# Kernel tuning notes

Hardware: AMD Instinct MI355X
Metric: run time of the kernel (lower is better)

## Reference

```python
import jax, jax.numpy as jnp
import numpy as np

B, N, D, T, L = 16, 64, 4, 40, 10
H, K = 128, 4
E = N * (N - 1)


def setup_inputs() -> dict:
    key = jax.random.key(0)
    ks = jax.random.split(key, 24)
    s = 0.05
    off = np.ones((N, N)) - np.eye(N)
    recv, send = np.where(off)  # rel_rec one-hot of recv, rel_send one-hot of send
    p = {}
    p["data"] = jax.random.normal(ks[0], (B, N, D, T), jnp.float32)
    p["rel_type"] = jax.random.uniform(ks[1], (B, E, K), dtype=jnp.float32)
    p["msg_W1"] = jax.random.normal(ks[2], (K, 2 * H, H), jnp.float32) * s
    p["msg_b1"] = jnp.zeros((K, H), jnp.float32)
    p["msg_W2"] = jax.random.normal(ks[3], (K, H, H), jnp.float32) * s
    p["msg_b2"] = jnp.zeros((K, H), jnp.float32)
    p["Wr_h"] = jax.random.normal(ks[4], (H, H), jnp.float32) * s
    p["Wi_h"] = jax.random.normal(ks[5], (H, H), jnp.float32) * s
    p["Wh_h"] = jax.random.normal(ks[6], (H, H), jnp.float32) * s
    p["Wr_in"] = jax.random.normal(ks[7], (D, H), jnp.float32) * s
    p["br_in"] = jnp.zeros((H,), jnp.float32)
    p["Wi_in"] = jax.random.normal(ks[8], (D, H), jnp.float32) * s
    p["bi_in"] = jnp.zeros((H,), jnp.float32)
    p["Wn_in"] = jax.random.normal(ks[9], (D, H), jnp.float32) * s
    p["bn_in"] = jnp.zeros((H,), jnp.float32)
    p["Wo1"] = jax.random.normal(ks[10], (H, H), jnp.float32) * s
    p["bo1"] = jnp.zeros((H,), jnp.float32)
    p["Wo2"] = jax.random.normal(ks[11], (H, H), jnp.float32) * s
    p["bo2"] = jnp.zeros((H,), jnp.float32)
    p["Wo3"] = jax.random.normal(ks[12], (H, D), jnp.float32) * s
    p["bo3"] = jnp.zeros((D,), jnp.float32)
    p["recv_idx"] = jnp.asarray(recv, jnp.int32)
    p["send_idx"] = jnp.asarray(send, jnp.int32)
    return p


def _forward(data, rel_type, msg_W1, msg_b1, msg_W2, msg_b2, Wr_h, Wi_h, Wh_h,
             Wr_in, br_in, Wi_in, bi_in, Wn_in, bn_in,
             Wo1, bo1, Wo2, bo2, Wo3, bo3, recv_idx, send_idx):
    inputs = jnp.transpose(data, (0, 3, 1, 2))  # [B,T,N,D]
    Bv = inputs.shape[0]

    def single_step(ins, hidden):
        # gather == matmul with one-hot rel_send / rel_rec
        pre_msg = jnp.concatenate([hidden[:, send_idx], hidden[:, recv_idx]], axis=-1)  # [B,E,2H]
        m = jnp.tanh(jnp.einsum('bef,kfh->bkeh', pre_msg, msg_W1) + msg_b1[None, :, None, :])
        m = jnp.tanh(jnp.einsum('bkeh,khg->bkeg', m, msg_W2) + msg_b2[None, :, None, :])
        # sum over edge types weighted by rel_type, normalized by num edge types
        all_msgs = jnp.einsum('bkeh,bek->beh', m, rel_type) / K
        # scatter-add to receivers == rel_rec^T matmul; normalized by n_in_node
        agg = jnp.zeros((Bv, N, H), all_msgs.dtype).at[:, recv_idx].add(all_msgs) / D
        r = jax.nn.sigmoid(ins @ Wr_in + br_in + agg @ Wr_h)
        i = jax.nn.sigmoid(ins @ Wi_in + bi_in + agg @ Wi_h)
        n = jnp.tanh(ins @ Wn_in + bn_in + r * (agg @ Wh_h))
        hidden = (1.0 - i) * n + i * hidden
        y = jax.nn.relu(hidden @ Wo1 + bo1)
        y = jax.nn.relu(y @ Wo2 + bo2)
        pred = ins + y @ Wo3 + bo3
        return pred, hidden

    inputs_pad = jnp.concatenate([inputs, jnp.zeros((Bv, L, N, D), inputs.dtype)], axis=1)
    xs_t = jnp.transpose(inputs_pad, (1, 0, 2, 3))  # [T+L,B,N,D]

    def scan_fn(carry, xs):
        hidden, prev = carry
        step, x_t = xs
        ins = jnp.where(step < T, x_t, prev)  # burn-in then closed-loop
        pred, hidden = single_step(ins, hidden)
        return (hidden, pred), pred

    init = (jnp.zeros((Bv, N, H), jnp.float32), jnp.zeros((Bv, N, D), jnp.float32))
    _, preds = jax.lax.scan(scan_fn, init, (jnp.arange(T + L), xs_t))
    preds = jnp.transpose(preds, (1, 2, 3, 0))  # [B,N,D,T+L]
    return preds[..., -L:]


def reference(data, rel_type, msg_W1, msg_b1, msg_W2, msg_b2, Wr_h, Wi_h, Wh_h,
              Wr_in, br_in, Wi_in, bi_in, Wn_in, bn_in,
              Wo1, bo1, Wo2, bo2, Wo3, bo3, recv_idx, send_idx):
    return _forward(data, rel_type, msg_W1, msg_b1, msg_W2, msg_b2, Wr_h, Wi_h, Wh_h,
                    Wr_in, br_in, Wi_in, bi_in, Wn_in, bn_in,
                    Wo1, bo1, Wo2, bo2, Wo3, bo3, recv_idx, send_idx)
```

## Files before the change

### kernel.cpp

```cpp
#include <hip/hip_runtime.h>
#include <hip/hip_bf16.h>
#include <math.h>

#define Bb 16
#define Nn 64
#define Dd 4
#define Tt 40
#define Ll 10
#define Hh 128
#define Kk 4
#define Ee (Nn*(Nn-1))
#define BNH (Bb*Nn*Hh)
#define SIGMA 2.8853900817779268f

typedef __attribute__((ext_vector_type(8))) short short8;
typedef __attribute__((ext_vector_type(4))) float f32x4;

#define AS1 __attribute__((address_space(1)))
#define AS3 __attribute__((address_space(3)))

__device__ __forceinline__ float tanhE(float y){
    float e = __builtin_amdgcn_exp2f(y);
    float r = __builtin_amdgcn_rcpf(e + 1.0f);
    return fmaf(-2.0f, r, 1.0f);
}
__device__ __forceinline__ float tanh_fast(float x){ return tanhE(SIGMA * x); }
__device__ __forceinline__ float sigmoid_fast(float x){
    return __builtin_amdgcn_rcpf(1.0f + __expf(-x));
}
__device__ __forceinline__ unsigned short f2bf(float x){
    unsigned int u = __float_as_uint(x);
    return (unsigned short)((u + 0x7FFFu + ((u >> 16) & 1u)) >> 16);
}
__device__ __forceinline__ unsigned int pack_bf2(float lo, float hi){
    union { __hip_bfloat162 h; unsigned int u; } cv;
    cv.h = __float22bfloat162_rn(make_float2(lo, hi));
    return cv.u;
}
__device__ __forceinline__ void g2lds16(const void* g, void* l){
    __builtin_amdgcn_global_load_lds((const AS1 unsigned int*)g,
                                     (AS3 unsigned int*)l, 16, 0, 0);
}

__global__ void __launch_bounds__(256) kW2f(const float* __restrict__ W2,
                                            const float* __restrict__ b2,
                                            unsigned short* __restrict__ W2f,
                                            float* __restrict__ b2l){
    if (blockIdx.x == 32){
        int i = threadIdx.x;
        b2l[i]       = SIGMA * b2[i];
        b2l[i + 256] = SIGMA * b2[i + 256];
        return;
    }
    int t    = blockIdx.x * 256 + threadIdx.x;
    int lane = t & 63;
    int nt   = (t >> 6) & 7;
    int kc   = (t >> 9) & 3;
    int k    = (t >> 11) & 3;
    int col  = nt * 16 + (lane & 15);
    int fb   = kc * 32 + (lane >> 4) * 8;
    unsigned int w[4];
#pragma unroll
    for (int p = 0; p < 4; ++p){
        unsigned short lo = f2bf(W2[(k*Hh + fb + 2*p    )*Hh + col]);
        unsigned short hi = f2bf(W2[(k*Hh + fb + 2*p + 1)*Hh + col]);
        w[p] = (unsigned int)lo | ((unsigned int)hi << 16);
    }
    ((uint4*)W2f)[t] = make_uint4(w[0], w[1], w[2], w[3]);
}

__global__ void __launch_bounds__(256) kW1f(const float* __restrict__ W1,
                                            unsigned short* __restrict__ W1f){
    int t    = blockIdx.x * 256 + threadIdx.x;
    int lane = t & 63;
    int nt   = (t >> 6) & 7;
    int kc   = (t >> 9) & 3;
    int s    = t >> 11;
    int col  = nt * 16 + (lane & 15);
    int fb   = kc * 32 + (lane >> 4) * 8;
    unsigned int w[4];
#pragma unroll
    for (int p = 0; p < 4; ++p){
        unsigned short lo = f2bf(W1[(size_t)(s*Hh + fb + 2*p    )*Hh + col]);
        unsigned short hi = f2bf(W1[(size_t)(s*Hh + fb + 2*p + 1)*Hh + col]);
        w[p] = (unsigned int)lo | ((unsigned int)hi << 16);
    }
    ((uint4*)W1f)[t] = make_uint4(w[0], w[1], w[2], w[3]);
}

__global__ void __launch_bounds__(256) kInit(const float* __restrict__ b1,
                                             float* __restrict__ Sf,
                                             float* __restrict__ Rr){
    int i = blockIdx.x*256 + threadIdx.x;
    Sf[i] = 0.0f;
    Rr[i] = SIGMA * b1[((i >> 13) & 3)*Hh + (i & 127)];
}

__global__ void __launch_bounds__(256) kA(const unsigned short* __restrict__ hbf,
                                          const unsigned short* __restrict__ W1f,
                                          const float* __restrict__ b1,
                                          float* __restrict__ Sf,
                                          float* __restrict__ Rr){
    const int blk   = blockIdx.x;
    const int bk    = blk & 63;
    const int b     = bk >> 2;
    const int k     = bk & 3;
    const int inner = blk >> 6;
    const int sr    = inner >> 1;
    const int mh    = inner & 1;
    const int s     = k*2 + sr;
    const int tid  = threadIdx.x;
    const int wave = tid >> 6;
    const int lane = tid & 63;
    const int nt0  = wave * 2;

    const short8* hv = (const short8*)hbf;
    const short8* wv = (const short8*)W1f;

    short8 a[2][4], bf[2][4];
#pragma unroll
    for (int m = 0; m < 2; ++m)
#pragma unroll
        for (int kc = 0; kc < 4; ++kc)
            a[m][kc] = hv[((size_t)((b*4 + mh*2 + m)*4) + kc)*64 + lane];
#pragma unroll
    for (int n = 0; n < 2; ++n)
#pragma unroll
        for (int kc = 0; kc < 4; ++kc)
            bf[n][kc] = wv[((size_t)(s*4 + kc)*8 + nt0 + n)*64 + lane];

    f32x4 acc[2][2];
#pragma unroll
    for (int m = 0; m < 2; ++m){ acc[m][0] = (f32x4)0.0f; acc[m][1] = (f32x4)0.0f; }

#pragma unroll
    for (int kc = 0; kc < 4; ++kc)
#pragma unroll
        for (int m = 0; m < 2; ++m){
            acc[m][0] = __builtin_amdgcn_mfma_f32_16x16x32_bf16(a[m][kc], bf[0][kc], acc[m][0], 0, 0, 0);
            acc[m][1] = __builtin_amdgcn_mfma_f32_16x16x32_bf16(a[m][kc], bf[1][kc], acc[m][1], 0, 0, 0);
        }

    const int col = lane & 15;
    const int r0  = (lane >> 4) << 2;
#pragma unroll
    for (int n = 0; n < 2; ++n){
        const int h  = (nt0 + n)*16 + col;
        const float bv = (sr == 1) ? b1[k*Hh + h] : 0.0f;
#pragma unroll
        for (int m = 0; m < 2; ++m){
            const int Mt = mh*2 + m;
#pragma unroll
            for (int r = 0; r < 4; ++r){
                const int node = Mt*16 + r0 + r;
                const float v = SIGMA*(acc[m][n][r] + bv);
                if (sr == 0)
                    Sf[((size_t)((b*4+k)*16 + (h>>3)))*512 + node*8 + (h&7)] = v;
                else
                    Rr[((size_t)((b*4+k)*64 + node))*128 + h] = v;
            }
        }
    }
}

__global__ void __launch_bounds__(256) kB(const float* __restrict__ Sf,
                                          const float* __restrict__ Rr,
                                          const unsigned short* __restrict__ W2f,
                                          const float* __restrict__ b2l,
                                          const float* __restrict__ rel,
                                          const int*   __restrict__ send_idx,
                                          float* __restrict__ aggp){
    __shared__ unsigned short w2s[32*512];
    __shared__ float rel_s[4][64];
    __shared__ float b2s[Hh];
    __shared__ float redu[4][4][Hh];

    const int blk  = blockIdx.x;
    const int bk   = blk & 63;
    const int nq   = blk >> 6;
    const int b    = bk >> 2;
    const int k    = bk & 3;
    const int n0   = nq * 4;
    const int tid  = threadIdx.x;
    const int wave = tid >> 6;
    const int lane = tid & 63;

    {
        const uint4* src = (const uint4*)(W2f + (size_t)k*16384);
        uint4* dst = (uint4*)w2s;
#pragma unroll
        for (int i = 0; i < 8; ++i)
            g2lds16(src + tid + i*256, dst + tid + i*256);
    }
    {
        int g = tid >> 6, e = tid & 63;
        rel_s[g][e] = (e < 63) ? rel[(b*Ee + (n0+g)*63 + e)*Kk + k] : 0.0f;
    }
    if (tid < 128) b2s[tid] = b2l[k*Hh + tid];
    __syncthreads();

    const int e  = wave*16 + (lane & 15);
    const int fo = lane >> 4;
    const float* SfB = Sf + (size_t)((b*4 + k)*16)*512;

    const int re   = wave*16 + ((lane >> 4) << 2);
    const int colb = lane & 15;
    const short8* w2v = (const short8*)w2s;

#pragma unroll
    for (int ph = 0; ph < 2; ++ph){
        short8 a0[4], a1[4];
#pragma unroll
        for (int n = 0; n < 2; ++n){
            const int nn = n0 + ph*2 + n;
            int srow = 0; if (e < 63) srow = send_idx[nn*63 + e];
            const float* Rp = Rr + (size_t)((b*4 + k)*64 + nn)*128;
#pragma unroll
            for (int kc = 0; kc < 4; ++kc){
                const int fg = kc*4 + fo;
                const float4* sv = (const float4*)(SfB + fg*512 + srow*8);
                const float4* rv = (const float4*)(Rp + fg*8);
                float4 s0 = sv[0], s1 = sv[1];
                float4 r0 = rv[0], r1 = rv[1];
                union { short8 v; unsigned int u[4]; } av;
                av.u[0] = pack_bf2(tanhE(s0.x+r0.x), tanhE(s0.y+r0.y));
                av.u[1] = pack_bf2(tanhE(s0.z+r0.z), tanhE(s0.w+r0.w));
                av.u[2] = pack_bf2(tanhE(s1.x+r1.x), tanhE(s1.y+r1.y));
                av.u[3] = pack_bf2(tanhE(s1.z+r1.z), tanhE(s1.w+r1.w));
                if (n == 0) a0[kc] = av.v; else a1[kc] = av.v;
            }
        }

        f32x4 acc0[8], acc1[8];
#pragma unroll
        for (int nt = 0; nt < 8; ++nt){ acc0[nt] = (f32x4)0.0f; acc1[nt] = (f32x4)0.0f; }
#pragma unroll
        for (int kc = 0; kc < 4; ++kc){
#pragma unroll
            for (int nt = 0; nt < 8; ++nt){
                short8 bfr = w2v[(kc*8 + nt)*64 + lane];
                acc0[nt] = __builtin_amdgcn_mfma_f32_16x16x32_bf16(a0[kc], bfr, acc0[nt], 0, 0, 0);
                acc1[nt] = __builtin_amdgcn_mfma_f32_16x16x32_bf16(a1[kc], bfr, acc1[nt], 0, 0, 0);
            }
        }

#pragma unroll
        for (int n = 0; n < 2; ++n){
            const float* relp = rel_s[ph*2 + n];
#pragma unroll
            for (int nt = 0; nt < 8; ++nt){
                f32x4 ac = (n == 0) ? acc0[nt] : acc1[nt];
                float bv = b2s[nt*16 + colb];
                float s = 0.0f;
#pragma unroll
                for (int r = 0; r < 4; ++r)
                    s = fmaf(relp[re + r], tanhE(fmaf(SIGMA, ac[r], bv)), s);
                s += __shfl_xor(s, 16);
                s += __shfl_xor(s, 32);
                if (lane < 16) redu[wave][ph*2 + n][nt*16 + lane] = s;
            }
        }
    }

    __syncthreads();
#pragma unroll
    for (int i = 0; i < 2; ++i){
        int idx = tid + i*256;
        int rcv = idx >> 7, h = idx & 127;
        float v = redu[0][rcv][h] + redu[1][rcv][h] + redu[2][rcv][h] + redu[3][rcv][h];
        aggp[(size_t)k*BNH + (size_t)(b*64 + n0 + rcv)*Hh + h] = v;
    }
}

__global__ void __launch_bounds__(128) kC(const float* __restrict__ data,
                                          const float* __restrict__ aggp,
                                          float* __restrict__ hidden,
                                          float* __restrict__ prevpred,
                                          unsigned short* __restrict__ hbf,
                                          const float* __restrict__ Wr_in, const float* __restrict__ br_in,
                                          const float* __restrict__ Wi_in, const float* __restrict__ bi_in,
                                          const float* __restrict__ Wn_in, const float* __restrict__ bn_in,
                                          const float* __restrict__ Wr_h,  const float* __restrict__ Wi_h,
                                          const float* __restrict__ Wh_h,
                                          const float* __restrict__ Wo1,   const float* __restrict__ bo1,
                                          const float* __restrict__ Wo2,   const float* __restrict__ bo2,
                                          const float* __restrict__ Wo3,   const float* __restrict__ bo3,
                                          float* __restrict__ out, int t){
    __shared__ float aggL[4][Hh];
    __shared__ float buf[4][Hh];
    __shared__ float insL[4][Dd];

    const int bn0 = blockIdx.x * 4;
    const int h   = threadIdx.x;

#pragma unroll
    for (int g = 0; g < 4; ++g){
        int bn = bn0 + g;
        aggL[g][h] = (aggp[bn*Hh + h] + aggp[BNH + bn*Hh + h] +
                      aggp[2*BNH + bn*Hh + h] + aggp[3*BNH + bn*Hh + h]) * (1.0f/16.0f);
    }
    if (h < 16){
        int g = h >> 2, d = h & 3;
        int bn = bn0 + g;
        insL[g][d] = (t < Tt) ? data[(bn*Dd + d)*Tt + t] : prevpred[bn*Dd + d];
    }
    __syncthreads();

    float rh[4] = {0,0,0,0}, ih[4] = {0,0,0,0}, hh[4] = {0,0,0,0};
    for (int f = 0; f < Hh; ++f){
        float wr = Wr_h[f*Hh + h], wi = Wi_h[f*Hh + h], wh = Wh_h[f*Hh + h];
#pragma unroll
        for (int g = 0; g < 4; ++g){
            float av = aggL[g][f];
            rh[g] += av*wr; ih[g] += av*wi; hh[g] += av*wh;
        }
    }

    const float wr0 = Wr_in[h],        wr1 = Wr_in[Hh + h],
                wr2 = Wr_in[2*Hh + h], wr3 = Wr_in[3*Hh + h];
    const float wi0 = Wi_in[h],        wi1 = Wi_in[Hh + h],
                wi2 = Wi_in[2*Hh + h], wi3 = Wi_in[3*Hh + h];
    const float wn0 = Wn_in[h],        wn1 = Wn_in[Hh + h],
                wn2 = Wn_in[2*Hh + h], wn3 = Wn_in[3*Hh + h];
    const float brv = br_in[h], biv = bi_in[h], bnv = bn_in[h];

    const int kc  = h >> 5;
    const int lhi = (h >> 3) & 3;
    const int j   = h & 7;

#pragma unroll
    for (int g = 0; g < 4; ++g){
        float i0 = insL[g][0], i1 = insL[g][1], i2 = insL[g][2], i3 = insL[g][3];
        float r  = sigmoid_fast(brv + i0*wr0 + i1*wr1 + i2*wr2 + i3*wr3 + rh[g]);
        float ii = sigmoid_fast(biv + i0*wi0 + i1*wi1 + i2*wi2 + i3*wi3 + ih[g]);
        float nn = tanh_fast   (bnv + i0*wn0 + i1*wn1 + i2*wn2 + i3*wn3 + r*hh[g]);
        float hold = hidden[(bn0+g)*Hh + h];
        float hnew = (1.0f - ii)*nn + ii*hold;
        hidden[(bn0+g)*Hh + h] = hnew;
        buf[g][h] = hnew;
        int bn   = bn0 + g;
        int bb   = bn >> 6, node64 = bn & 63;
        int Mt   = node64 >> 4;
        int lane = (node64 & 15) + lhi*16;
        hbf[((size_t)((bb*4 + Mt)*4 + kc)*64 + lane)*8 + j] = f2bf(hnew);
    }
    __syncthreads();

    float y1[4]; const float b1v = bo1[h];
#pragma unroll
    for (int g = 0; g < 4; ++g) y1[g] = b1v;
    for (int f = 0; f < Hh; ++f){
        float wv = Wo1[f*Hh + h];
#pragma unroll
        for (int g = 0; g < 4; ++g) y1[g] += buf[g][f]*wv;
    }
    __syncthreads();
#pragma unroll
    for (int g = 0; g < 4; ++g) buf[g][h] = fmaxf(y1[g], 0.0f);
    __syncthreads();

    float y2[4]; const float b2v = bo2[h];
#pragma unroll
    for (int g = 0; g < 4; ++g) y2[g] = b2v;
    for (int f = 0; f < Hh; ++f){
        float wv = Wo2[f*Hh + h];
#pragma unroll
        for (int g = 0; g < 4; ++g) y2[g] += buf[g][f]*wv;
    }
    __syncthreads();
#pragma unroll
    for (int g = 0; g < 4; ++g) buf[g][h] = fmaxf(y2[g], 0.0f);
    __syncthreads();

    if (h < 16){
        int g = h >> 2, d = h & 3;
        float pv = bo3[d];
        for (int f = 0; f < Hh; ++f) pv += buf[g][f]*Wo3[f*Dd + d];
        pv += insL[g][d];
        int bn = bn0 + g;
        prevpred[bn*Dd + d] = pv;
        if (t >= Tt) out[(bn*Dd + d)*Ll + (t - Tt)] = pv;
    }
}

extern "C" void kernel_launch(void* const* d_in, const int* in_sizes, int n_in,
                              void* d_out, int out_size, void* d_ws, size_t ws_size,
                              hipStream_t stream){
    const float* data  = (const float*)d_in[0];
    const float* rel   = (const float*)d_in[1];
    const float* W1    = (const float*)d_in[2];
    const float* b1    = (const float*)d_in[3];
    const float* W2    = (const float*)d_in[4];
    const float* b2    = (const float*)d_in[5];
    const float* Wr_h  = (const float*)d_in[6];
    const float* Wi_h  = (const float*)d_in[7];
    const float* Wh_h  = (const float*)d_in[8];
    const float* Wr_in = (const float*)d_in[9];
    const float* br_in = (const float*)d_in[10];
    const float* Wi_in = (const float*)d_in[11];
    const float* bi_in = (const float*)d_in[12];
    const float* Wn_in = (const float*)d_in[13];
    const float* bn_in = (const float*)d_in[14];
    const float* Wo1   = (const float*)d_in[15];
    const float* bo1   = (const float*)d_in[16];
    const float* Wo2   = (const float*)d_in[17];
    const float* bo2   = (const float*)d_in[18];
    const float* Wo3   = (const float*)d_in[19];
    const float* bo3   = (const float*)d_in[20];
    const int* send_idx = (const int*)d_in[22];

    float* out = (float*)d_out;
    float* ws  = (float*)d_ws;

    float* hidden   = ws;
    float* prevpred = hidden + BNH;
    float* Sf       = prevpred + Bb*Nn*Dd;
    float* Rr       = Sf + Bb*Kk*16*Nn*8;
    float* aggp     = Rr + Bb*Kk*Nn*Hh;
    unsigned short* W2f = (unsigned short*)(aggp + 4*BNH);
    float* b2l      = (float*)(W2f + 65536);
    unsigned short* W1f = (unsigned short*)(b2l + 512);
    unsigned short* hbf = W1f + 131072;

    hipMemsetAsync(hidden, 0, (Bb*Nn*Hh + Bb*Nn*Dd)*sizeof(float), stream);
    kW2f<<<33, 256, 0, stream>>>(W2, b2, W2f, b2l);
    kW1f<<<64, 256, 0, stream>>>(W1, W1f);
    kInit<<<2048, 256, 0, stream>>>(b1, Sf, Rr);

    for (int t = 0; t < Tt + Ll; ++t){
        kB<<<1024, 256, 0, stream>>>(Sf, Rr, W2f, b2l, rel, send_idx, aggp);
        kC<<<256, 128, 0, stream>>>(data, aggp, hidden, prevpred, hbf,
                                    Wr_in, br_in, Wi_in, bi_in, Wn_in, bn_in,
                                    Wr_h, Wi_h, Wh_h,
                                    Wo1, bo1, Wo2, bo2, Wo3, bo3, out, t);
        if (t < Tt + Ll - 1)
            kA<<<256, 256, 0, stream>>>(hbf, W1f, b1, Sf, Rr);
    }
}
```

Baseline: 2.360 ms.

## Assign one receiver per wave in kB, dropping send_idx gather and LDS reduction

```diff
diff --git a/kernel.cpp b/kernel.cpp
--- a/kernel.cpp
+++ b/kernel.cpp
@@ -168,12 +168,10 @@
                                           const unsigned short* __restrict__ W2f,
                                           const float* __restrict__ b2l,
                                           const float* __restrict__ rel,
-                                          const int*   __restrict__ send_idx,
                                           float* __restrict__ aggp){
     __shared__ unsigned short w2s[32*512];
     __shared__ float rel_s[4][64];
     __shared__ float b2s[Hh];
-    __shared__ float redu[4][4][Hh];
 
     const int blk  = blockIdx.x;
     const int bk   = blk & 63;
@@ -193,82 +191,80 @@
             g2lds16(src + tid + i*256, dst + tid + i*256);
     }
     {
-        int g = tid >> 6, e = tid & 63;
-        rel_s[g][e] = (e < 63) ? rel[(b*Ee + (n0+g)*63 + e)*Kk + k] : 0.0f;
+        int g = tid >> 6, s = tid & 63;
+        int n = n0 + g;
+        float w = 0.0f;
+        if (s != n){
+            int e = s - (s > n);
+            w = rel[(b*Ee + n*63 + e)*Kk + k];
+        }
+        rel_s[g][s] = w;
     }
     if (tid < 128) b2s[tid] = b2l[k*Hh + tid];
     __syncthreads();
 
-    const int e  = wave*16 + (lane & 15);
-    const int fo = lane >> 4;
+    const int n    = n0 + wave;
+    const int fo   = lane >> 4;
+    const int srow = lane & 15;
     const float* SfB = Sf + (size_t)((b*4 + k)*16)*512;
-
-    const int re   = wave*16 + ((lane >> 4) << 2);
-    const int colb = lane & 15;
+    const float* Rp  = Rr + (size_t)((b*4 + k)*64 + n)*128;
     const short8* w2v = (const short8*)w2s;
-
-#pragma unroll
-    for (int ph = 0; ph < 2; ++ph){
-        short8 a0[4], a1[4];
-#pragma unroll
-        for (int n = 0; n < 2; ++n){
-            const int nn = n0 + ph*2 + n;
-            int srow = 0; if (e < 63) srow = send_idx[nn*63 + e];
-            const float* Rp = Rr + (size_t)((b*4 + k)*64 + nn)*128;
-#pragma unroll
-            for (int kc = 0; kc < 4; ++kc){
-                const int fg = kc*4 + fo;
-                const float4* sv = (const float4*)(SfB + fg*512 + srow*8);
-                const float4* rv = (const float4*)(Rp + fg*8);
-                float4 s0 = sv[0], s1 = sv[1];
-                float4 r0 = rv[0], r1 = rv[1];
-                union { short8 v; unsigned int u[4]; } av;
-                av.u[0] = pack_bf2(tanhE(s0.x+r0.x), tanhE(s0.y+r0.y));
-                av.u[1] = pack_bf2(tanhE(s0.z+r0.z), tanhE(s0.w+r0.w));
-                av.u[2] = pack_bf2(tanhE(s1.x+r1.x), tanhE(s1.y+r1.y));
-                av.u[3] = pack_bf2(tanhE(s1.z+r1.z), tanhE(s1.w+r1.w));
-                if (n == 0) a0[kc] = av.v; else a1[kc] = av.v;
-            }
-        }
-
-        f32x4 acc0[8], acc1[8];
-#pragma unroll
-        for (int nt = 0; nt < 8; ++nt){ acc0[nt] = (f32x4)0.0f; acc1[nt] = (f32x4)0.0f; }
+    const float* relw = rel_s[wave];
+
+    const int colb  = lane & 15;
+    const int rbase = (lane >> 4) << 2;
+
+    float aggacc[8];
+#pragma unroll
+    for (int nt = 0; nt < 8; ++nt) aggacc[nt] = 0.0f;
+
+#pragma unroll
+    for (int st = 0; st < 4; ++st){
+        short8 a[4];
+#pragma unroll
+        for (int kc = 0; kc < 4; ++kc){
+            const int fg = kc*4 + fo;
+            const float4* sv = (const float4*)(SfB + fg*512 + (st*16 + srow)*8);
+            const float4* rv = (const float4*)(Rp + fg*8);
+            float4 s0 = sv[0], s1 = sv[1];
+            float4 r0 = rv[0], r1 = rv[1];
+            union { short8 v; unsigned int u[4]; } av;
+            av.u[0] = pack_bf2(tanhE(s0.x+r0.x), tanhE(s0.y+r0.y));
+            av.u[1] = pack_bf2(tanhE(s0.z+r0.z), tanhE(s0.w+r0.w));
+            av.u[2] = pack_bf2(tanhE(s1.x+r1.x), tanhE(s1.y+r1.y));
+            av.u[3] = pack_bf2(tanhE(s1.z+r1.z), tanhE(s1.w+r1.w));
+            a[kc] = av.v;
+        }
+
+        f32x4 acc[8];
+#pragma unroll
+        for (int nt = 0; nt < 8; ++nt) acc[nt] = (f32x4)0.0f;
 #pragma unroll
         for (int kc = 0; kc < 4; ++kc){
 #pragma unroll
             for (int nt = 0; nt < 8; ++nt){
                 short8 bfr = w2v[(kc*8 + nt)*64 + lane];
-                acc0[nt] = __builtin_amdgcn_mfma_f32_16x16x32_bf16(a0[kc], bfr, acc0[nt], 0, 0, 0);
-                acc1[nt] = __builtin_amdgcn_mfma_f32_16x16x32_bf16(a1[kc], bfr, acc1[nt], 0, 0, 0);
+                acc[nt] = __builtin_amdgcn_mfma_f32_16x16x32_bf16(a[kc], bfr, acc[nt], 0, 0, 0);
             }
         }
 
 #pragma unroll
-        for (int n = 0; n < 2; ++n){
-            const float* relp = rel_s[ph*2 + n];
-#pragma unroll
-            for (int nt = 0; nt < 8; ++nt){
-                f32x4 ac = (n == 0) ? acc0[nt] : acc1[nt];
-                float bv = b2s[nt*16 + colb];
-                float s = 0.0f;
-#pragma unroll
-                for (int r = 0; r < 4; ++r)
-                    s = fmaf(relp[re + r], tanhE(fmaf(SIGMA, ac[r], bv)), s);
-                s += __shfl_xor(s, 16);
-                s += __shfl_xor(s, 32);
-                if (lane < 16) redu[wave][ph*2 + n][nt*16 + lane] = s;
-            }
-        }
-    }
-
-    __syncthreads();
-#pragma unroll
-    for (int i = 0; i < 2; ++i){
-        int idx = tid + i*256;
-        int rcv = idx >> 7, h = idx & 127;
-        float v = redu[0][rcv][h] + redu[1][rcv][h] + redu[2][rcv][h] + redu[3][rcv][h];
-        aggp[(size_t)k*BNH + (size_t)(b*64 + n0 + rcv)*Hh + h] = v;
+        for (int nt = 0; nt < 8; ++nt){
+            float bv = b2s[nt*16 + colb];
+            float s = 0.0f;
+#pragma unroll
+            for (int r = 0; r < 4; ++r)
+                s = fmaf(relw[st*16 + rbase + r], tanhE(fmaf(SIGMA, acc[nt][r], bv)), s);
+            s += __shfl_xor(s, 16);
+            s += __shfl_xor(s, 32);
+            aggacc[nt] += s;
+        }
+    }
+
+    if (lane < 16){
+#pragma unroll
+        for (int nt = 0; nt < 8; ++nt)
+            aggp[(size_t)k*BNH + (size_t)(b*64 + n)*Hh + nt*16 + lane] = aggacc[nt];
     }
 }
 
@@ -407,7 +403,6 @@
     const float* bo2   = (const float*)d_in[18];
     const float* Wo3   = (const float*)d_in[19];
     const float* bo3   = (const float*)d_in[20];
-    const int* send_idx = (const int*)d_in[22];
 
     float* out = (float*)d_out;
     float* ws  = (float*)d_ws;
@@ -428,7 +423,7 @@
     kInit<<<2048, 256, 0, stream>>>(b1, Sf, Rr);
 
     for (int t = 0; t < Tt + Ll; ++t){
-        kB<<<1024, 256, 0, stream>>>(Sf, Rr, W2f, b2l, rel, send_idx, aggp);
+        kB<<<1024, 256, 0, stream>>>(Sf, Rr, W2f, b2l, rel, aggp);
         kC<<<256, 128, 0, stream>>>(data, aggp, hidden, prevpred, hbf,
                                     Wr_in, br_in, Wi_in, bi_in, Wn_in, bn_in,
                                     Wr_h, Wi_h, Wh_h,
```

Result: slower. 2.448 ms (+3.7%).
